# Kernel tuning notes

Hardware: AMD Instinct MI355X
Metric: run time of the kernel (lower is better)

## Reference

```python
import jax, jax.numpy as jnp
import numpy as np

DEPTH = 10
LAMDA = 1e-3
EPS = 1e-7


def setup_inputs() -> dict:
    key = jax.random.key(0)
    k1, k2, k3, k4 = jax.random.split(key, 4)
    B, D, O = 16384, 512, 256
    N = 2 ** DEPTH - 1        # inner nodes
    L = 2 ** DEPTH            # leaves
    data = jax.random.normal(k1, (B, D), jnp.float32)
    # small scale on W keeps sigmoid away from saturation (like nn.Linear init)
    W = jax.random.normal(k2, (N, D + 1), jnp.float32) * 0.02
    beta = jax.random.normal(k3, (N,), jnp.float32)
    param = jax.random.normal(k4, (L, O), jnp.float32)
    return {"data": data, "W": W, "beta": beta, "param": param}


def reference(data, W, beta, param):
    B = data.shape[0]
    L = param.shape[0]
    # _data_augment_: prepend constant 1 as bias feature -> [B, D+1]
    x = jnp.concatenate([jnp.ones((B, 1), data.dtype), data], axis=1)
    # inner_nodes: sigmoid(beta * linear(x)) -> [B, N]
    p = jax.nn.sigmoid(beta * (x @ W.T))
    # per-node (go-left, go-right) probabilities -> [B, N, 2]
    path_prob = jnp.stack([p, 1.0 - p], axis=2)

    mu = jnp.ones((B, 1), data.dtype)          # path prob of root
    penalty = jnp.asarray(0.0, data.dtype)
    begin = 0
    for layer in range(DEPTH):                  # fixed small loop over depth
        n = 2 ** layer
        pp = path_prob[:, begin:begin + n, :].reshape(B, 2 * n)  # [B, 2n]
        mu_rep = jnp.repeat(mu, 2, axis=1)                        # [B, 2n]
        # vectorized form of the per-node penalty loop
        alpha = jnp.sum(pp * mu_rep, axis=0) / (jnp.sum(mu_rep, axis=0) + EPS)
        alpha = jnp.clip(alpha, EPS, 1.0 - EPS)
        coeff = LAMDA * (2.0 ** (-layer))
        penalty = penalty - coeff * 0.5 * jnp.sum(jnp.log(alpha) + jnp.log(1.0 - alpha))
        mu = mu_rep * pp
        begin += n

    # mu: [B, leaf_num]; leaf_nodes: mu @ softmax(param)
    dist = jax.nn.softmax(param, axis=1)       # [L, O]
    output = mu @ dist                          # [B, O]
    # greatest_path_probability: hard argmax leaf (one-hot @ dist == gather)
    ids = jnp.argmax(mu, axis=1)
    prediction = dist[ids]                      # [B, O]
    # LogProb=True
    return (jnp.log(prediction), jnp.log(output), penalty, W)
```

## Files before the change

kernel.cpp:

```cpp
#include <hip/hip_runtime.h>
#include <hip/hip_bf16.h>

#define B_ROWS 16384
#define DDIM   512
#define NNODES 1023
#define NLEAF  1024
#define ODIM   256
#define LAMDA  1e-3
#define EPSV   1e-7f

typedef __bf16 bf16x8v __attribute__((ext_vector_type(8)));
typedef _Float16 f16x8 __attribute__((ext_vector_type(8)));
typedef float  f32x16v __attribute__((ext_vector_type(16)));

__device__ __forceinline__ float bf2f(unsigned short u) {
    return __uint_as_float(((unsigned)u) << 16);
}

__device__ __forceinline__ void gload16h(const _Float16* g, _Float16* l) {
    __builtin_amdgcn_global_load_lds(
        (const __attribute__((address_space(1))) unsigned int*)g,
        (__attribute__((address_space(3))) unsigned int*)l, 16, 0, 0);
}
__device__ __forceinline__ void gload16b(const __hip_bfloat16* g, __hip_bfloat16* l) {
    __builtin_amdgcn_global_load_lds(
        (const __attribute__((address_space(1))) unsigned int*)g,
        (__attribute__((address_space(3))) unsigned int*)l, 16, 0, 0);
}

__global__ __launch_bounds__(256)
void prep_all(const float* __restrict__ data, const float* __restrict__ W,
              const float* __restrict__ param,
              _Float16* __restrict__ Dh, _Float16* __restrict__ Dl,
              _Float16* __restrict__ Wh, _Float16* __restrict__ Wl,
              float* __restrict__ outW,
              float* __restrict__ logdist, __hip_bfloat16* __restrict__ DT2)
{
    __shared__ float red[4], red2[4];
    if (blockIdx.x < 4096) {
        int idx = blockIdx.x * 256 + threadIdx.x;
        int b  = idx >> 6;
        int k8 = idx & 63;
        const float4 v0 = *reinterpret_cast<const float4*>(&data[(size_t)b * DDIM + k8 * 8]);
        const float4 v1 = *reinterpret_cast<const float4*>(&data[(size_t)b * DDIM + k8 * 8 + 4]);
        float a[8] = {v0.x, v0.y, v0.z, v0.w, v1.x, v1.y, v1.z, v1.w};
        __align__(16) _Float16 h[8], l[8];
#pragma unroll
        for (int j = 0; j < 8; ++j) {
            h[j] = (_Float16)a[j];
            l[j] = (_Float16)((a[j] - (float)h[j]) * 2048.f);
        }
        int by = b >> 8, tl = (b >> 5) & 7, ln = (b & 31) | ((k8 & 1) << 5), ks = k8 >> 1;
        size_t off = ((((size_t)by * 32 + ks) * 8 + tl) * 64 + ln) * 8;
        *reinterpret_cast<ulonglong2*>(&Dh[off]) = *reinterpret_cast<const ulonglong2*>(h);
        *reinterpret_cast<ulonglong2*>(&Dl[off]) = *reinterpret_cast<const ulonglong2*>(l);
    } else if (blockIdx.x < 4352) {
        int idx = (blockIdx.x - 4096) * 256 + threadIdx.x;
        int t  = idx & 255;
        int ks = (idx >> 8) & 31;
        int nb = idx >> 13;
        int tm = t >> 6, ln = t & 63;
        int node = nb * 128 + tm * 32 + (ln & 31);
        int k = ks * 16 + (ln >> 5) * 8;
        __align__(16) _Float16 h[8], l[8];
        if (node < NNODES) {
#pragma unroll
            for (int j = 0; j < 8; ++j) {
                float a = W[(size_t)node * 513 + 1 + k + j];
                h[j] = (_Float16)a;
                l[j] = (_Float16)((a - (float)h[j]) * 2048.f);
            }
        } else {
#pragma unroll
            for (int j = 0; j < 8; ++j) { h[j] = (_Float16)0.f; l[j] = (_Float16)0.f; }
        }
        size_t off = (size_t)idx * 8;
        *reinterpret_cast<ulonglong2*>(&Wh[off]) = *reinterpret_cast<const ulonglong2*>(h);
        *reinterpret_cast<ulonglong2*>(&Wl[off]) = *reinterpret_cast<const ulonglong2*>(l);
    } else if (blockIdx.x < 6404) {
        int i = (blockIdx.x - 4352) * 256 + threadIdx.x;
        if (i < NNODES * 513) outW[i] = W[i];
    } else {
        int l = blockIdx.x - 6404;
        int o = threadIdx.x;
        float x = param[(size_t)l * ODIM + o];
        float m = x;
#pragma unroll
        for (int s = 1; s < 64; s <<= 1) m = fmaxf(m, __shfl_xor(m, s, 64));
        if ((o & 63) == 0) red[o >> 6] = m;
        __syncthreads();
        m = fmaxf(fmaxf(red[0], red[1]), fmaxf(red[2], red[3]));
        float e = expf(x - m);
        float s = e;
#pragma unroll
        for (int k = 1; k < 64; k <<= 1) s += __shfl_xor(s, k, 64);
        if ((o & 63) == 0) red2[o >> 6] = s;
        __syncthreads();
        s = red2[0] + red2[1] + red2[2] + red2[3];
        float d = e / s;
        logdist[(size_t)l * ODIM + o] = logf(d);
        int kc = l >> 4, kk = l & 15;
        int lane = (o & 31) | ((kk >> 3) << 5);
        DT2[(((size_t)kc * 8 + (o >> 5)) * 64 + lane) * 8 + (kk & 7)] = __float2bfloat16(d);
    }
}

__global__ __launch_bounds__(512, 4)
void gemm1_mfma(const _Float16* __restrict__ Wh, const _Float16* __restrict__ Wl,
                const _Float16* __restrict__ Dh, const _Float16* __restrict__ Dl,
                const float* __restrict__ W, const float* __restrict__ beta,
                float* __restrict__ PT)
{
    __shared__ _Float16 lds[2][8192];
    const int tid = threadIdx.x;
    const int lane = tid & 63;
    const int wv = tid >> 6;
    const int wm = wv & 1, wn = wv >> 1;
    const int id = blockIdx.x;
    const int xcd = id & 7, slot = id >> 3;
    const int bx = slot & 7;
    const int by = xcd * 16 + (slot >> 3);
    const int by256 = by >> 1;
    const int tlb = (by & 1) * 4;

    const int q  = tid & 255;
    const int qt = q >> 6, qn = q & 63;
    const _Float16* Wsel = (tid < 256) ? Wh : Wl;
    const _Float16* Dsel = (tid < 256) ? Dh : Dl;
    const _Float16* wsrc = Wsel + (size_t)bx * 65536 + qt * 512 + qn * 8;
    const _Float16* dsrc = Dsel + (size_t)by256 * 131072 + (tlb + qt) * 512 + qn * 8;

    f32x16v acc_h[2] = {};
    f32x16v acc_l[2] = {};

#define STAGE(buf, ks) do { \
        gload16h(wsrc + (size_t)(ks) * 2048, &lds[buf][tid * 8]); \
        gload16h(dsrc + (size_t)(ks) * 4096, &lds[buf][4096 + tid * 8]); \
    } while (0)

    STAGE(0, 0);
    for (int t = 0; t < 32; ++t) {
        const int cur = t & 1;
        if (t < 31) {
            STAGE(cur ^ 1, t + 1);
            asm volatile("s_waitcnt vmcnt(2)" ::: "memory");
        } else {
            asm volatile("s_waitcnt vmcnt(0)" ::: "memory");
        }
        __builtin_amdgcn_s_barrier();

        f16x8 ah[2], al[2], bh, bl;
#pragma unroll
        for (int i = 0; i < 2; ++i) {
            int ao = ((wm * 2 + i) * 64 + lane) * 8;
            ah[i] = *reinterpret_cast<const f16x8*>(&lds[cur][ao]);
            al[i] = *reinterpret_cast<const f16x8*>(&lds[cur][2048 + ao]);
        }
        {
            int bo = (wn * 64 + lane) * 8;
            bh = *reinterpret_cast<const f16x8*>(&lds[cur][4096 + bo]);
            bl = *reinterpret_cast<const f16x8*>(&lds[cur][6144 + bo]);
        }
        __builtin_amdgcn_s_setprio(1);
#pragma unroll
        for (int i = 0; i < 2; ++i) {
            acc_h[i] = __builtin_amdgcn_mfma_f32_32x32x16_f16(ah[i], bh, acc_h[i], 0, 0, 0);
            acc_l[i] = __builtin_amdgcn_mfma_f32_32x32x16_f16(ah[i], bl, acc_l[i], 0, 0, 0);
            acc_l[i] = __builtin_amdgcn_mfma_f32_32x32x16_f16(al[i], bh, acc_l[i], 0, 0, 0);
        }
        __builtin_amdgcn_s_setprio(0);
        asm volatile("s_waitcnt lgkmcnt(0)" ::: "memory");
        __builtin_amdgcn_s_barrier();
    }
#undef STAGE

#pragma unroll
    for (int i = 0; i < 2; ++i) {
#pragma unroll
        for (int r = 0; r < 16; ++r) {
            int node = bx * 128 + wm * 64 + i * 32 + ((r & 3) + 8 * (r >> 2) + 4 * (lane >> 5));
            if (node < NNODES) {
                float w0 = W[(size_t)node * 513];
                float bt = beta[node];
                float z = acc_h[i][r] + acc_l[i][r] * 4.8828125e-4f;
                float s = bt * (z + w0);
                float p = 1.f / (1.f + expf(-s));
                PT[(size_t)node * B_ROWS + by * 128 + wn * 32 + (lane & 31)] = p;
            }
        }
    }
}

__global__ __launch_bounds__(256, 4)
void tree_pass(const float* __restrict__ PT,
               __hip_bfloat16* __restrict__ MU2,
               float* __restrict__ pval,
               int*   __restrict__ pidx)
{
    const int tid = threadIdx.x;
    const int rb = blockIdx.x & 63;
    const int g  = blockIdx.x >> 6;
    const int b  = rb * 256 + tid;

    const int c4 = 15 + g;
    const int n3 = (c4 - 1) >> 1;
    const int n2 = (n3 - 1) >> 1;
    const int n1 = (n2 - 1) >> 1;
    const float pc4 = PT[(size_t)c4 * B_ROWS + b];
    const float pn3 = PT[(size_t)n3 * B_ROWS + b];
    const float pn2 = PT[(size_t)n2 * B_ROWS + b];
    const float pn1 = PT[(size_t)n1 * B_ROWS + b];
    const float pn0 = PT[b];
    float pre = ((c4 & 1) ? pn3 : 1.f - pn3)
              * ((n3 & 1) ? pn2 : 1.f - pn2)
              * ((n2 & 1) ? pn1 : 1.f - pn1)
              * ((n1 & 1) ? pn0 : 1.f - pn0);
    float root[2] = { pre * pc4, pre * (1.f - pc4) };

    __align__(16) __hip_bfloat16 mbv[64];
    float bestv = -1.f; int besti = 0;
#pragma unroll
    for (int ss = 0; ss < 2; ++ss) {
        const int t = 2 * g + ss;
        float s[32];
#pragma unroll
        for (int u = 1; u < 32; ++u) {
            int lvl = 31 - __clz(u);
            int node = ((32 << lvl) - 1) + t * (1 << lvl) + (u - (1 << lvl));
            s[u] = PT[(size_t)node * B_ROWS + b];
        }
        float w[64];
        w[1] = root[ss];
#pragma unroll
        for (int u = 1; u < 32; ++u) {
            w[2 * u]     = w[u] * s[u];
            w[2 * u + 1] = w[u] * (1.f - s[u]);
        }
#pragma unroll
        for (int q = 0; q < 32; ++q) {
            float lv = w[32 + q];
            mbv[ss * 32 + q] = __float2bfloat16(lv);
            if (lv > bestv) { bestv = lv; besti = t * 32 + q; }
        }
    }
    {
        const int mb_ = b >> 7, mt_ = (b >> 5) & 3, lnlo = b & 31;
        const ulonglong2* src = reinterpret_cast<const ulonglong2*>(mbv);
#pragma unroll
        for (int c = 0; c < 4; ++c) {
            size_t base16 = (((size_t)mb_ * 64 + g * 4 + c) * 4 + mt_) * 64;
            *reinterpret_cast<ulonglong2*>(&MU2[(base16 + lnlo) * 8])      = src[c * 2];
            *reinterpret_cast<ulonglong2*>(&MU2[(base16 + 32 + lnlo) * 8]) = src[c * 2 + 1];
        }
    }
    pval[(size_t)g * B_ROWS + b] = bestv;
    pidx[(size_t)g * B_ROWS + b] = besti;
}

__global__ __launch_bounds__(256)
void colsum_argmax(const __hip_bfloat16* __restrict__ MU2, float* __restrict__ partial,
                   const float* __restrict__ pval, const int* __restrict__ pidx,
                   const float* __restrict__ logdist, float* __restrict__ out0)
{
    __shared__ float red[4][2][8];
    __shared__ int sid[64];
    const int t = threadIdx.x;
    if (blockIdx.x < 256) {
        const int blk = blockIdx.x;
        const int kc = blk >> 2, mbg = blk & 3;
        const int w = t >> 6, ln = t & 63;
        float a[8] = {0.f, 0.f, 0.f, 0.f, 0.f, 0.f, 0.f, 0.f};
        for (int it = 0; it < 32; ++it) {
            int it2 = it * 4 + w;
            int mb = mbg * 32 + (it2 >> 2), mt = it2 & 3;
            size_t a16 = (((size_t)mb * 64 + kc) * 4 + mt) * 64 + ln;
            ulonglong2 u = *reinterpret_cast<const ulonglong2*>(&MU2[a16 * 8]);
            const unsigned short* hs = reinterpret_cast<const unsigned short*>(&u);
#pragma unroll
            for (int j = 0; j < 8; ++j) a[j] += bf2f(hs[j]);
        }
#pragma unroll
        for (int m = 1; m < 32; m <<= 1)
#pragma unroll
            for (int j = 0; j < 8; ++j) a[j] += __shfl_xor(a[j], m, 64);
        if ((ln & 31) == 0) {
#pragma unroll
            for (int j = 0; j < 8; ++j) red[w][ln >> 5][j] = a[j];
        }
        __syncthreads();
        if (t < 16) {
            float s = red[0][t >> 3][t & 7] + red[1][t >> 3][t & 7]
                    + red[2][t >> 3][t & 7] + red[3][t >> 3][t & 7];
            partial[(size_t)mbg * NLEAF + kc * 16 + t] = s;
        }
    } else {
        const int blk = blockIdx.x - 256;
        if (t < 64) {
            int row = blk * 64 + t;
            float bv = -1.f; int bi = 0;
            for (int g = 0; g < 16; ++g) {
                float v = pval[(size_t)g * B_ROWS + row];
                if (v > bv) { bv = v; bi = pidx[(size_t)g * B_ROWS + row]; }
            }
            sid[t] = bi;
        }
        __syncthreads();
        for (int rr = 0; rr < 64; ++rr) {
            int id = sid[rr];
            out0[(size_t)(blk * 64 + rr) * ODIM + t] = logdist[(size_t)id * ODIM + t];
        }
    }
}

__global__ __launch_bounds__(256)
void gemm2_penalty(const __hip_bfloat16* __restrict__ MU2,
                   const __hip_bfloat16* __restrict__ DT2,
                   float* __restrict__ out1,
                   const float* __restrict__ partial, float* __restrict__ out_pen)
{
    __shared__ __hip_bfloat16 ldsA[2][2048];
    __shared__ __hip_bfloat16 ldsB[2][8192];
    __shared__ float M[2048];
    __shared__ double dred[256];
    const int tid = threadIdx.x;
    if (blockIdx.x == 256) {
        for (int i = tid; i < 1024; i += 256)
            M[1024 + i] = partial[i] + partial[NLEAF + i] + partial[2 * NLEAF + i] + partial[3 * NLEAF + i];
        __syncthreads();
        for (int n = 512; n >= 1; n >>= 1) {
            for (int u = n + tid; u < 2 * n; u += 256) M[u] = M[2 * u] + M[2 * u + 1];
            __syncthreads();
        }
        double acc = 0.0;
        for (int u = 2 + tid; u < 2048; u += 256) {
            int lvl = 31 - __clz(u);
            float a = M[u] / (M[u >> 1] + EPSV);
            a = fminf(fmaxf(a, EPSV), 1.f - EPSV);
            float term = logf(a) + logf(1.f - a);
            acc -= ldexp((double)LAMDA * 0.5, 1 - lvl) * (double)term;
        }
        dred[tid] = acc;
        __syncthreads();
        for (int s = 128; s > 0; s >>= 1) {
            if (tid < s) dred[tid] += dred[tid + s];
            __syncthreads();
        }
        if (tid == 0) out_pen[0] = (float)dred[0];
        return;
    }
    const int lane = tid & 63;
    const int w = tid >> 6;
    const int blk = blockIdx.x;
    const int m0 = blk * 64;
    const int mb = blk >> 1;
    const int mtbase = (blk & 1) * 2;
    const int s_kcl = tid >> 7, s_mti = (tid >> 6) & 1, s_ln = tid & 63;

    f32x16v acc[2][2] = {};

#define STAGE2(buf, kc0) do { \
        size_t sa16 = (((size_t)mb * 64 + (kc0) + s_kcl) * 4 + mtbase + s_mti) * 64 + s_ln; \
        gload16b(MU2 + sa16 * 8, &ldsA[buf][tid * 8]); \
        gload16b(DT2 + ((size_t)(kc0) * 512 + tid) * 8,             &ldsB[buf][tid * 8]); \
        gload16b(DT2 + ((size_t)(kc0) * 512 + 256 + tid) * 8,       &ldsB[buf][2048 + tid * 8]); \
        gload16b(DT2 + ((size_t)((kc0) + 1) * 512 + tid) * 8,       &ldsB[buf][4096 + tid * 8]); \
        gload16b(DT2 + ((size_t)((kc0) + 1) * 512 + 256 + tid) * 8, &ldsB[buf][6144 + tid * 8]); \
    } while (0)

    STAGE2(0, 0);
    for (int it = 0; it < 32; ++it) {
        const int cur = it & 1;
        if (it + 1 < 32) {
            STAGE2(cur ^ 1, 2 * (it + 1));
            asm volatile("s_waitcnt vmcnt(5)" ::: "memory");
        } else {
            asm volatile("s_waitcnt vmcnt(0)" ::: "memory");
        }
        __builtin_amdgcn_s_barrier();
        bf16x8v a[2][2], bb[2][2];
#pragma unroll
        for (int kcl = 0; kcl < 2; ++kcl)
#pragma unroll
            for (int i = 0; i < 2; ++i) {
                a[kcl][i]  = *reinterpret_cast<const bf16x8v*>(&ldsA[cur][((kcl * 2 + i) * 64 + lane) * 8]);
                bb[kcl][i] = *reinterpret_cast<const bf16x8v*>(&ldsB[cur][((kcl * 8 + 2 * w + i) * 64 + lane) * 8]);
            }
        __builtin_amdgcn_s_setprio(1);
#pragma unroll
        for (int kcl = 0; kcl < 2; ++kcl)
#pragma unroll
            for (int i = 0; i < 2; ++i)
#pragma unroll
                for (int j = 0; j < 2; ++j)
                    acc[i][j] = __builtin_amdgcn_mfma_f32_32x32x16_bf16(a[kcl][i], bb[kcl][j], acc[i][j], 0, 0, 0);
        __builtin_amdgcn_s_setprio(0);
        asm volatile("s_waitcnt lgkmcnt(0)" ::: "memory");
        __builtin_amdgcn_s_barrier();
    }
#undef STAGE2
#pragma unroll
    for (int i = 0; i < 2; ++i)
#pragma unroll
        for (int j = 0; j < 2; ++j)
#pragma unroll
            for (int r = 0; r < 16; ++r) {
                int row = m0 + i * 32 + (r & 3) + 8 * (r >> 2) + 4 * (lane >> 5);
                int col = w * 64 + j * 32 + (lane & 31);
                out1[(size_t)row * ODIM + col] = logf(acc[i][j][r]);
            }
}

extern "C" void kernel_launch(void* const* d_in, const int* in_sizes, int n_in,
                              void* d_out, int out_size, void* d_ws, size_t ws_size,
                              hipStream_t stream)
{
    (void)in_sizes; (void)n_in; (void)out_size; (void)ws_size;
    const float* data  = (const float*)d_in[0];
    const float* W     = (const float*)d_in[1];
    const float* beta  = (const float*)d_in[2];
    const float* param = (const float*)d_in[3];
    float* out = (float*)d_out;

    char* ws = (char*)d_ws;
    size_t off = 0;
    float* PT = (float*)(ws + off);                   off += (size_t)NNODES * B_ROWS * 4;
    char* X = ws + off;                               off += 2 * 1048576 + 2 * 16777216;
    _Float16* Wh = (_Float16*)(X);
    _Float16* Wl = (_Float16*)(X + 1048576);
    _Float16* Dh = (_Float16*)(X + 2 * 1048576);
    _Float16* Dl = (_Float16*)(X + 2 * 1048576 + 16777216);
    __hip_bfloat16* MU2 = (__hip_bfloat16*)(X + 2 * 1048576);
    __hip_bfloat16* DT2 = (__hip_bfloat16*)(ws + off); off += (size_t)ODIM * NLEAF * 2;
    float* logdist = (float*)(ws + off);              off += (size_t)NLEAF * ODIM * 4;
    float* partial = (float*)(ws + off);              off += (size_t)4 * NLEAF * 4;
    float* pval    = (float*)(ws + off);              off += (size_t)16 * B_ROWS * 4;
    int*   pidx    = (int*)(ws + off);                off += (size_t)16 * B_ROWS * 4;

    float* out_logpred = out;
    float* out_logout  = out + (size_t)B_ROWS * ODIM;
    float* out_pen     = out + 2 * (size_t)B_ROWS * ODIM;
    float* out_W       = out_pen + 1;

    prep_all<<<7428, 256, 0, stream>>>(data, W, param, Dh, Dl, Wh, Wl, out_W, logdist, DT2);

    gemm1_mfma<<<1024, 512, 0, stream>>>(Wh, Wl, Dh, Dl, W, beta, PT);

    tree_pass<<<1024, 256, 0, stream>>>(PT, MU2, pval, pidx);

    colsum_argmax<<<512, 256, 0, stream>>>(MU2, partial, pval, pidx, logdist, out_logpred);

    gemm2_penalty<<<257, 256, 0, stream>>>(MU2, DT2, out_logout, partial, out_pen);
}
```

Before: 151.0 us.

## Fuse leaf column sums into tree pass via LDS reduction and atomics

Moves the per-leaf column-sum reduction out of a separate kernel that re-read the bf16 MU2 buffer and into tree_pass. Leaf probabilities are summed in shared memory while still held in fp32 and accumulated with global atomicAdd into a zeroed leafsum array. The kernels are then reorganised: gemm2 runs alone, and a finalize kernel does the argmax gather plus the penalty. This removes one full pass over MU2 but adds barriers and LDS traffic inside tree_pass, plus a memset and non-deterministic atomic ordering.

After: 151.6 us. No clear change (+0.4%).

```diff
diff --git a/kernel.cpp b/kernel.cpp
--- a/kernel.cpp
+++ b/kernel.cpp
@@ -195,8 +195,11 @@
 void tree_pass(const float* __restrict__ PT,
                __hip_bfloat16* __restrict__ MU2,
                float* __restrict__ pval,
-               int*   __restrict__ pidx)
-{
+               int*   __restrict__ pidx,
+               float* __restrict__ leafsum)
+{
+    __shared__ float cs[32][257];
+    __shared__ float ps[32][8];
     const int tid = threadIdx.x;
     const int rb = blockIdx.x & 63;
     const int g  = blockIdx.x >> 6;
@@ -242,6 +245,24 @@
             mbv[ss * 32 + q] = __float2bfloat16(lv);
             if (lv > bestv) { bestv = lv; besti = t * 32 + q; }
         }
+#pragma unroll
+        for (int q = 0; q < 32; ++q) cs[q][tid] = w[32 + q];
+        __syncthreads();
+        {
+            const int q = tid & 31, seg = tid >> 5;
+            float sum = 0.f;
+#pragma unroll
+            for (int r = 0; r < 32; ++r) sum += cs[q][seg * 32 + r];
+            ps[q][seg] = sum;
+        }
+        __syncthreads();
+        if (tid < 32) {
+            float tot = 0.f;
+#pragma unroll
+            for (int sg = 0; sg < 8; ++sg) tot += ps[tid][sg];
+            atomicAdd(&leafsum[t * 32 + tid], tot);
+        }
+        __syncthreads();
     }
     {
         const int mb_ = b >> 7, mt_ = (b >> 5) & 3, lnlo = b & 31;
@@ -258,96 +279,63 @@
 }
 
 __global__ __launch_bounds__(256)
-void colsum_argmax(const __hip_bfloat16* __restrict__ MU2, float* __restrict__ partial,
-                   const float* __restrict__ pval, const int* __restrict__ pidx,
-                   const float* __restrict__ logdist, float* __restrict__ out0)
-{
-    __shared__ float red[4][2][8];
+void finalize(const float* __restrict__ pval, const int* __restrict__ pidx,
+              const float* __restrict__ logdist, float* __restrict__ out0,
+              const float* __restrict__ leafsum, float* __restrict__ out_pen)
+{
     __shared__ int sid[64];
-    const int t = threadIdx.x;
-    if (blockIdx.x < 256) {
-        const int blk = blockIdx.x;
-        const int kc = blk >> 2, mbg = blk & 3;
-        const int w = t >> 6, ln = t & 63;
-        float a[8] = {0.f, 0.f, 0.f, 0.f, 0.f, 0.f, 0.f, 0.f};
-        for (int it = 0; it < 32; ++it) {
-            int it2 = it * 4 + w;
-            int mb = mbg * 32 + (it2 >> 2), mt = it2 & 3;
-            size_t a16 = (((size_t)mb * 64 + kc) * 4 + mt) * 64 + ln;
-            ulonglong2 u = *reinterpret_cast<const ulonglong2*>(&MU2[a16 * 8]);
-            const unsigned short* hs = reinterpret_cast<const unsigned short*>(&u);
-#pragma unroll
-            for (int j = 0; j < 8; ++j) a[j] += bf2f(hs[j]);
-        }
-#pragma unroll
-        for (int m = 1; m < 32; m <<= 1)
-#pragma unroll
-            for (int j = 0; j < 8; ++j) a[j] += __shfl_xor(a[j], m, 64);
-        if ((ln & 31) == 0) {
-#pragma unroll
-            for (int j = 0; j < 8; ++j) red[w][ln >> 5][j] = a[j];
-        }
-        __syncthreads();
-        if (t < 16) {
-            float s = red[0][t >> 3][t & 7] + red[1][t >> 3][t & 7]
-                    + red[2][t >> 3][t & 7] + red[3][t >> 3][t & 7];
-            partial[(size_t)mbg * NLEAF + kc * 16 + t] = s;
-        }
-    } else {
-        const int blk = blockIdx.x - 256;
-        if (t < 64) {
-            int row = blk * 64 + t;
-            float bv = -1.f; int bi = 0;
-            for (int g = 0; g < 16; ++g) {
-                float v = pval[(size_t)g * B_ROWS + row];
-                if (v > bv) { bv = v; bi = pidx[(size_t)g * B_ROWS + row]; }
-            }
-            sid[t] = bi;
-        }
-        __syncthreads();
-        for (int rr = 0; rr < 64; ++rr) {
-            int id = sid[rr];
-            out0[(size_t)(blk * 64 + rr) * ODIM + t] = logdist[(size_t)id * ODIM + t];
-        }
-    }
-}
-
-__global__ __launch_bounds__(256)
-void gemm2_penalty(const __hip_bfloat16* __restrict__ MU2,
-                   const __hip_bfloat16* __restrict__ DT2,
-                   float* __restrict__ out1,
-                   const float* __restrict__ partial, float* __restrict__ out_pen)
-{
-    __shared__ __hip_bfloat16 ldsA[2][2048];
-    __shared__ __hip_bfloat16 ldsB[2][8192];
     __shared__ float M[2048];
     __shared__ double dred[256];
-    const int tid = threadIdx.x;
+    const int t = threadIdx.x;
     if (blockIdx.x == 256) {
-        for (int i = tid; i < 1024; i += 256)
-            M[1024 + i] = partial[i] + partial[NLEAF + i] + partial[2 * NLEAF + i] + partial[3 * NLEAF + i];
+        for (int i = t; i < 1024; i += 256) M[1024 + i] = leafsum[i];
         __syncthreads();
         for (int n = 512; n >= 1; n >>= 1) {
-            for (int u = n + tid; u < 2 * n; u += 256) M[u] = M[2 * u] + M[2 * u + 1];
+            for (int u = n + t; u < 2 * n; u += 256) M[u] = M[2 * u] + M[2 * u + 1];
             __syncthreads();
         }
         double acc = 0.0;
-        for (int u = 2 + tid; u < 2048; u += 256) {
+        for (int u = 2 + t; u < 2048; u += 256) {
             int lvl = 31 - __clz(u);
             float a = M[u] / (M[u >> 1] + EPSV);
             a = fminf(fmaxf(a, EPSV), 1.f - EPSV);
             float term = logf(a) + logf(1.f - a);
             acc -= ldexp((double)LAMDA * 0.5, 1 - lvl) * (double)term;
         }
-        dred[tid] = acc;
+        dred[t] = acc;
         __syncthreads();
         for (int s = 128; s > 0; s >>= 1) {
-            if (tid < s) dred[tid] += dred[tid + s];
+            if (t < s) dred[t] += dred[t + s];
             __syncthreads();
         }
-        if (tid == 0) out_pen[0] = (float)dred[0];
+        if (t == 0) out_pen[0] = (float)dred[0];
         return;
     }
+    const int blk = blockIdx.x;
+    if (t < 64) {
+        int row = blk * 64 + t;
+        float bv = -1.f; int bi = 0;
+        for (int g = 0; g < 16; ++g) {
+            float v = pval[(size_t)g * B_ROWS + row];
+            if (v > bv) { bv = v; bi = pidx[(size_t)g * B_ROWS + row]; }
+        }
+        sid[t] = bi;
+    }
+    __syncthreads();
+    for (int rr = 0; rr < 64; ++rr) {
+        int id = sid[rr];
+        out0[(size_t)(blk * 64 + rr) * ODIM + t] = logdist[(size_t)id * ODIM + t];
+    }
+}
+
+__global__ __launch_bounds__(256)
+void gemm2_log(const __hip_bfloat16* __restrict__ MU2,
+               const __hip_bfloat16* __restrict__ DT2,
+               float* __restrict__ out1)
+{
+    __shared__ __hip_bfloat16 ldsA[2][2048];
+    __shared__ __hip_bfloat16 ldsB[2][8192];
+    const int tid = threadIdx.x;
     const int lane = tid & 63;
     const int w = tid >> 6;
     const int blk = blockIdx.x;
@@ -432,7 +420,7 @@
     __hip_bfloat16* MU2 = (__hip_bfloat16*)(X + 2 * 1048576);
     __hip_bfloat16* DT2 = (__hip_bfloat16*)(ws + off); off += (size_t)ODIM * NLEAF * 2;
     float* logdist = (float*)(ws + off);              off += (size_t)NLEAF * ODIM * 4;
-    float* partial = (float*)(ws + off);              off += (size_t)4 * NLEAF * 4;
+    float* leafsum = (float*)(ws + off);              off += (size_t)NLEAF * 4;
     float* pval    = (float*)(ws + off);              off += (size_t)16 * B_ROWS * 4;
     int*   pidx    = (int*)(ws + off);                off += (size_t)16 * B_ROWS * 4;
 
@@ -441,13 +429,14 @@
     float* out_pen     = out + 2 * (size_t)B_ROWS * ODIM;
     float* out_W       = out_pen + 1;
 
+    hipMemsetAsync(leafsum, 0, NLEAF * 4, stream);
     prep_all<<<7428, 256, 0, stream>>>(data, W, param, Dh, Dl, Wh, Wl, out_W, logdist, DT2);
 
     gemm1_mfma<<<1024, 512, 0, stream>>>(Wh, Wl, Dh, Dl, W, beta, PT);
 
-    tree_pass<<<1024, 256, 0, stream>>>(PT, MU2, pval, pidx);
-
-    colsum_argmax<<<512, 256, 0, stream>>>(MU2, partial, pval, pidx, logdist, out_logpred);
-
-    gemm2_penalty<<<257, 256, 0, stream>>>(MU2, DT2, out_logout, partial, out_pen);
-}
+    tree_pass<<<1024, 256, 0, stream>>>(PT, MU2, pval, pidx, leafsum);
+
+    gemm2_log<<<256, 256, 0, stream>>>(MU2, DT2, out_logout);
+
+    finalize<<<257, 256, 0, stream>>>(pval, pidx, logdist, out_logpred, leafsum, out_pen);
+}
```
